# Performance work log

Measured on AMD Instinct MI355X. Metric: run time of the kernel, lower is better.

Reference implementation:

```python
import jax, jax.numpy as jnp
import numpy as np
from jax import lax

B, S, D, H = 64, 256, 512, 8
DH = D // H
FILTER_HEIGHTS = (1, 3, 5)


def setup_inputs() -> dict:
    key = jax.random.key(0)
    ks = jax.random.split(key, 20)
    w = lambda k, shape, s=0.02: (jax.random.normal(k, shape, dtype=jnp.float32) * s)
    inp = {
        "x": jax.random.normal(ks[0], (B, S, D), dtype=jnp.float32),
        "particles": jax.random.uniform(ks[1], (B, S, 3), dtype=jnp.float32),
        # QKV and output projections
        "wq": w(ks[2], (D, D)),
        "wk": w(ks[3], (D, D)),
        "wv": w(ks[4], (D, D)),
        "dense_w": w(ks[5], (D, D)),
        "dense_b": jnp.zeros((D,), jnp.float32),
        # attention-score smoothing convs: kernel (h, S, 1, 1) HWIO, full-width
        "conv1_k": w(ks[6], (1, S, 1, 1)),
        "conv1_b": jnp.zeros((1,), jnp.float32),
        "conv3_k": w(ks[7], (3, S, 1, 1)),
        "conv3_b": jnp.zeros((1,), jnp.float32),
        "conv5_k": w(ks[8], (5, S, 1, 1)),
        "conv5_b": jnp.zeros((1,), jnp.float32),
        # pairwise-feature mask net (1x1 convs == per-pair MLP): 4->8->8->1
        "mw1": w(ks[9], (4, 8), 0.1),
        "mb1": jnp.zeros((8,), jnp.float32),
        "mw2": w(ks[10], (8, 8), 0.1),
        "mb2": jnp.zeros((8,), jnp.float32),
        "mw3": w(ks[11], (8, 1), 0.1),
        "mb3": jnp.zeros((1,), jnp.float32),
    }
    return inp


def _conv_same(x, kern, bias):
    # x: [N, S, S, 1], kern: [h, S, 1, 1] -> [N, S, S, 1], TF 'same' padding, stride 1
    y = lax.conv_general_dilated(x, kern, window_strides=(1, 1), padding="SAME",
                                 dimension_numbers=("NHWC", "HWIO", "NHWC"))
    return y + bias


def _pairwise_features(particles):
    pt, eta, phi = particles[..., 0], particles[..., 1], particles[..., 2]
    pt_i, pt_j = pt[:, :, None], pt[:, None, :]
    d_eta = eta[:, :, None] - eta[:, None, :]
    dp = phi[:, :, None] - phi[:, None, :]
    d_phi = jnp.arctan2(jnp.sin(dp), jnp.cos(dp))
    delta = jnp.sqrt(d_eta ** 2 + d_phi ** 2)
    min_pt = jnp.minimum(pt_i, pt_j)
    kT = min_pt * delta
    z = min_pt / (pt_i + pt_j + 1e-8)
    m2 = jnp.maximum(pt_i ** 2 + pt_j ** 2 - 2.0 * pt_i * pt_j * jnp.cos(d_phi), 1e-8)
    eps = 1e-8
    return jnp.stack([
        jnp.log(jnp.maximum(delta, eps)),
        jnp.log(jnp.maximum(kT, eps)),
        jnp.log(jnp.maximum(z, eps)),
        jnp.log(m2),
    ], axis=-1)  # [B, S, S, 4]


def reference(x, particles, wq, wk, wv, dense_w, dense_b,
              conv1_k, conv1_b, conv3_k, conv3_b, conv5_k, conv5_b,
              mw1, mb1, mw2, mb2, mw3, mb3):
    b = x.shape[0]
    split = lambda t: t.reshape(b, S, H, DH).transpose(0, 2, 1, 3)  # [B,H,S,DH]
    q, k, v = split(x @ wq), split(x @ wk), split(x @ wv)

    scores = jnp.einsum("bhqd,bhkd->bhqk", q, k) / jnp.sqrt(jnp.float32(DH))

    # conv smoothing over score matrices (avg of full-width convs h in {1,3,5})
    xs = scores.reshape(b * H, S, S, 1)
    c1 = _conv_same(xs, conv1_k, conv1_b)
    c3 = _conv_same(xs, conv3_k, conv3_b)
    c5 = _conv_same(xs, conv5_k, conv5_b)
    scores = ((c1 + c3 + c5) / 3.0).reshape(b, H, S, S)

    # pairwise-feature mask (1x1 conv net == per-pair MLP)
    feats = _pairwise_features(particles)               # [B,S,S,4]
    m = jax.nn.relu(feats @ mw1 + mb1)
    m = jax.nn.relu(m @ mw2 + mb2)
    m = (m @ mw3 + mb3)[..., 0]                         # [B,S,S]
    m = jnp.clip(m, -10.0, 10.0)
    scores = scores + m[:, None, :, :]

    weights = jax.nn.softmax(scores, axis=-1)
    attn = jnp.einsum("bhqk,bhkd->bhqd", weights, v)
    concat = attn.transpose(0, 2, 1, 3).reshape(b, S, D)
    return concat @ dense_w + dense_b
```

## Files before the change

### kernel.cpp

```cpp
#include <hip/hip_runtime.h>
#include <hip/hip_bf16.h>
#include <math.h>

#define B   64
#define S   256
#define DD  512
#define H   8
#define DH  64
#define BH  (B*H)

typedef short s16x8 __attribute__((ext_vector_type(8)));
typedef short s16x4 __attribute__((ext_vector_type(4)));
typedef float f32x4 __attribute__((ext_vector_type(4)));

typedef __attribute__((address_space(3))) unsigned int       lds_u32;
typedef __attribute__((address_space(1))) const unsigned int glb_u32;

__device__ __forceinline__ short f2bf(float f) {
    __bf16 h = (__bf16)f;
    union { __bf16 b; short s; } u; u.b = h;
    return u.s;
}

__device__ __forceinline__ void glds16(const void* g, void* l) {
    __builtin_amdgcn_global_load_lds((glb_u32*)g, (lds_u32*)l, 16, 0, 0);
}

__global__ __launch_bounds__(256) void convert_x_kernel(
    const float* __restrict__ x, ushort* __restrict__ xbf)
{
    const int idx = blockIdx.x * 256 + threadIdx.x;
    const float4 f0 = *(const float4*)(x + (size_t)idx * 8);
    const float4 f1 = *(const float4*)(x + (size_t)idx * 8 + 4);
    s16x8 o = { f2bf(f0.x), f2bf(f0.y), f2bf(f0.z), f2bf(f0.w),
                f2bf(f1.x), f2bf(f1.y), f2bf(f1.z), f2bf(f1.w) };
    *(s16x8*)(xbf + (size_t)idx * 8) = o;
}

__global__ __launch_bounds__(256) void transpose_w_kernel(
    const float* __restrict__ wq, const float* __restrict__ wk,
    const float* __restrict__ wv, const float* __restrict__ wd,
    ushort* __restrict__ wt)
{
    __shared__ float tile[32][33];
    const int z = blockIdx.z;
    const float* w = (z == 0) ? wq : (z == 1) ? wk : (z == 2) ? wv : wd;
    const int k0 = blockIdx.y * 32, n0 = blockIdx.x * 32;
    const int tx = threadIdx.x & 31, ty = threadIdx.x >> 5;

    #pragma unroll
    for (int r = 0; r < 32; r += 8)
        tile[ty + r][tx] = w[(size_t)(k0 + ty + r) * DD + n0 + tx];
    __syncthreads();
    #pragma unroll
    for (int r = 0; r < 32; r += 8)
        wt[(size_t)z * DD * DD + (size_t)(n0 + ty + r) * DD + k0 + tx] =
            (ushort)f2bf(tile[tx][ty + r]);
}

__global__ __launch_bounds__(256) void build_toeplitz_frag_kernel(
    const float* __restrict__ c1k, const float* __restrict__ c3k,
    const float* __restrict__ c5k, ushort* __restrict__ btf)
{
    const int idx  = blockIdx.x * 256 + threadIdx.x;
    const int lane = idx & 63;
    const int st   = (idx >> 6) % 40;
    const int n    = idx / (40 * 64);
    const int c    = n * 16 + (lane & 15);
    const int r    = st >> 3;
    const int tb   = (st & 7) * 32 + (lane >> 4) * 8;

    s16x8 o;
    #pragma unroll
    for (int e = 0; e < 8; ++e) {
        const int ki = tb + e - c + 127;
        float val = 0.f;
        if (ki >= 0 && ki < 256) {
            val = c5k[r * 256 + ki];
            if (r >= 1 && r <= 3) val += c3k[(r - 1) * 256 + ki];
            if (r == 2)           val += c1k[ki];
            val *= (1.f / 24.f);
        }
        o[e] = f2bf(val);
    }
    *(s16x8*)(btf + (size_t)idx * 8) = o;
}

__global__ __launch_bounds__(256) void vfrag_repack_kernel(
    const ushort* __restrict__ vbT, ushort* __restrict__ vfrag)
{
    const int idx  = blockIdx.x * 256 + threadIdx.x;
    const int lane = idx & 63;
    const int kk   = (idx >> 6) & 7;
    const int n    = (idx >> 9) & 3;
    const int head = idx >> 11;
    const s16x8 v = *(const s16x8*)(vbT
        + ((size_t)(head * 64 + n * 16 + (lane & 15))) * 256
        + kk * 32 + (lane >> 4) * 8);
    *(s16x8*)(vfrag + (size_t)idx * 8) = v;
}

__global__ __launch_bounds__(256) void gemm_vT_kernel(
    const ushort* __restrict__ A, const ushort* __restrict__ Bt,
    ushort* __restrict__ vo)
{
    __shared__ ushort As[128 * 64];
    __shared__ ushort Bs[128 * 64];

    const int tid  = threadIdx.x;
    const int lane = tid & 63, w = tid >> 6;
    const int l15  = lane & 15, l4 = lane >> 4;
    const int wr   = w >> 1, wc = w & 1;
    const int row0 = blockIdx.y * 128, col0 = blockIdx.x * 128;

    f32x4 acc[4][4];
    #pragma unroll
    for (int mt = 0; mt < 4; ++mt)
        #pragma unroll
        for (int nt = 0; nt < 4; ++nt)
            acc[mt][nt] = (f32x4){0.f, 0.f, 0.f, 0.f};

    const int arow = tid >> 3;
    const int acol = (tid & 7) * 8;
    char* ldsA = (char*)As + (tid >> 6) * 1024;
    char* ldsB = (char*)Bs + (tid >> 6) * 1024;

    for (int k0 = 0; k0 < DD; k0 += 64) {
        #pragma unroll
        for (int i = 0; i < 4; ++i)
            glds16(A  + (size_t)(row0 + arow + 32 * i) * DD + k0 + acol,
                   ldsA + 4096 * i);
        #pragma unroll
        for (int i = 0; i < 4; ++i)
            glds16(Bt + (size_t)(col0 + arow + 32 * i) * DD + k0 + acol,
                   ldsB + 4096 * i);
        __syncthreads();

        #pragma unroll
        for (int kk = 0; kk < 2; ++kk) {
            s16x8 af[4], bf[4];
            #pragma unroll
            for (int mt = 0; mt < 4; ++mt) {
                const int row = wr * 64 + mt * 16 + l15;
                af[mt] = *(const s16x8*)((char*)As + row * 128 + kk * 64 + l4 * 16);
            }
            #pragma unroll
            for (int nt = 0; nt < 4; ++nt) {
                const int col = wc * 64 + nt * 16 + l15;
                bf[nt] = *(const s16x8*)((char*)Bs + col * 128 + kk * 64 + l4 * 16);
            }
            #pragma unroll
            for (int mt = 0; mt < 4; ++mt)
                #pragma unroll
                for (int nt = 0; nt < 4; ++nt)
                    acc[mt][nt] = __builtin_amdgcn_mfma_f32_16x16x32_bf16(
                                      af[mt], bf[nt], acc[mt][nt], 0, 0, 0);
        }
        __syncthreads();
    }

    #pragma unroll
    for (int mt = 0; mt < 4; ++mt)
        #pragma unroll
        for (int nt = 0; nt < 4; ++nt) {
            const int r = row0 + wr * 64 + mt * 16 + l4 * 4;
            const int c = col0 + wc * 64 + nt * 16 + l15;
            const int bb = r >> 8, ss = r & 255;
            const int hh = c >> 6, dd = c & 63;
            s16x4 pk = { f2bf(acc[mt][nt][0]), f2bf(acc[mt][nt][1]),
                         f2bf(acc[mt][nt][2]), f2bf(acc[mt][nt][3]) };
            *(s16x4*)(vo + ((size_t)((bb * H + hh) * DH + dd)) * S + ss) = pk;
        }
}

template<int MODE>
__global__ __launch_bounds__(256) void gemm_swapped_kernel(
    const ushort* __restrict__ WtAll, const ushort* __restrict__ Tok,
    ushort* __restrict__ qo, ushort* __restrict__ ko,
    const float* __restrict__ bias, float* __restrict__ outf)
{
    __shared__ ushort As[128 * 64];
    __shared__ ushort Bs[128 * 64];

    const int tid  = threadIdx.x;
    const int lane = tid & 63, w = tid >> 6;
    const int l15  = lane & 15, l4 = lane >> 4;
    const int wr   = w >> 1, wc = w & 1;
    const int frow0 = blockIdx.y * 128;
    const int trow0 = blockIdx.x * 128;
    const ushort* A = WtAll + (MODE == 0 ? (size_t)blockIdx.z * DD * DD : 0);

    f32x4 acc[4][4];
    #pragma unroll
    for (int mt = 0; mt < 4; ++mt)
        #pragma unroll
        for (int nt = 0; nt < 4; ++nt)
            acc[mt][nt] = (f32x4){0.f, 0.f, 0.f, 0.f};

    const int arow = tid >> 3;
    const int acol = (tid & 7) * 8;
    char* ldsA = (char*)As + (tid >> 6) * 1024;
    char* ldsB = (char*)Bs + (tid >> 6) * 1024;

    for (int k0 = 0; k0 < DD; k0 += 64) {
        #pragma unroll
        for (int i = 0; i < 4; ++i)
            glds16(A   + (size_t)(frow0 + arow + 32 * i) * DD + k0 + acol,
                   ldsA + 4096 * i);
        #pragma unroll
        for (int i = 0; i < 4; ++i)
            glds16(Tok + (size_t)(trow0 + arow + 32 * i) * DD + k0 + acol,
                   ldsB + 4096 * i);
        __syncthreads();

        #pragma unroll
        for (int kk = 0; kk < 2; ++kk) {
            s16x8 af[4], bf[4];
            #pragma unroll
            for (int mt = 0; mt < 4; ++mt) {
                const int row = wr * 64 + mt * 16 + l15;
                af[mt] = *(const s16x8*)((char*)As + row * 128 + kk * 64 + l4 * 16);
            }
            #pragma unroll
            for (int nt = 0; nt < 4; ++nt) {
                const int col = wc * 64 + nt * 16 + l15;
                bf[nt] = *(const s16x8*)((char*)Bs + col * 128 + kk * 64 + l4 * 16);
            }
            #pragma unroll
            for (int mt = 0; mt < 4; ++mt)
                #pragma unroll
                for (int nt = 0; nt < 4; ++nt)
                    acc[mt][nt] = __builtin_amdgcn_mfma_f32_16x16x32_bf16(
                                      af[mt], bf[nt], acc[mt][nt], 0, 0, 0);
        }
        __syncthreads();
    }

    if (MODE == 0) {
        ushort* dst = (blockIdx.z == 0) ? qo : ko;
        #pragma unroll
        for (int mt = 0; mt < 4; ++mt)
            #pragma unroll
            for (int nt = 0; nt < 4; ++nt) {
                const int r = trow0 + wc * 64 + nt * 16 + l15;
                const int c = frow0 + wr * 64 + mt * 16 + l4 * 4;
                const int bb = r >> 8, ss = r & 255;
                const int hh = c >> 6, dd = c & 63;
                s16x4 pk = { f2bf(acc[mt][nt][0]), f2bf(acc[mt][nt][1]),
                             f2bf(acc[mt][nt][2]), f2bf(acc[mt][nt][3]) };
                *(s16x4*)(dst + (((size_t)(bb * H + hh)) * S + ss) * DH + dd) = pk;
            }
    } else {
        #pragma unroll
        for (int mt = 0; mt < 4; ++mt) {
            const int c = frow0 + wr * 64 + mt * 16 + l4 * 4;
            const float4 b4 = *(const float4*)(bias + c);
            #pragma unroll
            for (int nt = 0; nt < 4; ++nt) {
                const int r = trow0 + wc * 64 + nt * 16 + l15;
                float4 o = make_float4(acc[mt][nt][0] + b4.x, acc[mt][nt][1] + b4.y,
                                       acc[mt][nt][2] + b4.z, acc[mt][nt][3] + b4.w);
                *(float4*)(outf + (size_t)r * DD + c) = o;
            }
        }
    }
}

__global__ __launch_bounds__(256) void pairwise_mlp_kernel(
    const float* __restrict__ particles,
    const float* __restrict__ mw1, const float* __restrict__ mb1,
    const float* __restrict__ mw2, const float* __restrict__ mb2,
    const float* __restrict__ mw3, const float* __restrict__ mb3,
    const float* __restrict__ c1b, const float* __restrict__ c3b,
    const float* __restrict__ c5b,
    float* __restrict__ mfrag)
{
    __shared__ float w1[32], b1[8], w2[64], b2[8], w3[8];
    __shared__ float b3s;
    const int tid = threadIdx.x;
    if (tid < 32)                 w1[tid]        = mw1[tid];
    if (tid >= 32 && tid < 40)    b1[tid - 32]   = mb1[tid - 32];
    if (tid >= 64 && tid < 128)   w2[tid - 64]   = mw2[tid - 64];
    if (tid >= 128 && tid < 136)  b2[tid - 128]  = mb2[tid - 128];
    if (tid >= 136 && tid < 144)  w3[tid - 136]  = mw3[tid - 136];
    if (tid == 144)               b3s            = mb3[0];

    const int bi = blockIdx.x;
    const int bb = bi >> 8;
    const float pt_i  = particles[(size_t)bi * 3 + 0];
    const float eta_i = particles[(size_t)bi * 3 + 1];
    const float phi_i = particles[(size_t)bi * 3 + 2];

    const int j = tid;
    const float* pj = particles + ((size_t)(bb * S) + j) * 3;
    const float pt_j = pj[0], eta_j = pj[1], phi_j = pj[2];

    __syncthreads();

    const float d_eta = eta_i - eta_j;
    const float dp    = phi_i - phi_j;
    const float d_phi = dp - 6.28318530717958647692f
                             * rintf(dp * 0.15915494309189533577f);
    const float delta = sqrtf(d_eta * d_eta + d_phi * d_phi);
    const float min_pt = fminf(pt_i, pt_j);
    const float kT = min_pt * delta;
    const float zf = min_pt / (pt_i + pt_j + 1e-8f);
    const float cd = cosf(d_phi);
    const float m2 = fmaxf(pt_i * pt_i + pt_j * pt_j - 2.0f * pt_i * pt_j * cd, 1e-8f);

    const float eps = 1e-8f;
    const float f[4] = { logf(fmaxf(delta, eps)),
                         logf(fmaxf(kT,    eps)),
                         logf(fmaxf(zf,    eps)),
                         logf(m2) };

    float h1[8];
    #pragma unroll
    for (int o = 0; o < 8; ++o) {
        float s = b1[o];
        #pragma unroll
        for (int i4 = 0; i4 < 4; ++i4) s += f[i4] * w1[i4 * 8 + o];
        h1[o] = fmaxf(s, 0.0f);
    }
    float h2[8];
    #pragma unroll
    for (int o = 0; o < 8; ++o) {
        float s = b2[o];
        #pragma unroll
        for (int i8 = 0; i8 < 8; ++i8) s += h1[i8] * w2[i8 * 8 + o];
        h2[o] = fmaxf(s, 0.0f);
    }
    float mv = b3s;
    #pragma unroll
    for (int i8 = 0; i8 < 8; ++i8) mv += h2[i8] * w3[i8];
    mv = fminf(fmaxf(mv, -10.0f), 10.0f);
    mv += (c1b[0] + c3b[0] + c5b[0]) * (1.f / 3.f);

    const int ii     = bi & 255;
    const int chunk2 = ii >> 7;
    const int rem    = ii & 127;
    const int wr     = rem >> 6, rt = (rem >> 4) & 3, l4h = (rem >> 2) & 3, rg = rem & 3;
    const int wc     = j >> 6,   n2 = (j >> 4) & 3,  l15 = j & 15;
    const int lane   = l4h * 16 + l15;
    const int w8     = wr * 4 + wc;
    mfrag[((((size_t)(bb * 2 + chunk2)) * 8 + w8) * 64 + lane) * 64
          + rt * 16 + n2 * 4 + rg] = mv;
}

__global__ __launch_bounds__(512, 4) void fused_mfma_kernel(
    const ushort* __restrict__ q, const ushort* __restrict__ kbuf,
    const ushort* __restrict__ vfrag, const ushort* __restrict__ btf,
    const float* __restrict__ mfrag, ushort* __restrict__ attn)
{
    __shared__ __align__(16) char pool[75776];
    char* SC   = pool;
    char* PB   = pool;
    float* RED = (float*)(pool + 73728);

    const int tid  = threadIdx.x;
    const int lane = tid & 63;
    const int w    = tid >> 6;
    const int wr   = w >> 2, wc = w & 3;
    const int l15  = lane & 15, l4 = lane >> 4;
    const int head = blockIdx.y;
    const int bb   = head >> 3, hh = head & 7;
    const int i0   = blockIdx.x * 128;
    const int cb   = wc * 64;

    {
        const ushort* kb_h = kbuf + (size_t)head * S * DH;
        const ushort* qb_h = q    + (size_t)head * S * DH;
        const int ntiles = 5 - wr;
        const int tg0    = wr * 5;
        f32x4 sacc[4][5];
        #pragma unroll
        for (int mt = 0; mt < 4; ++mt)
            #pragma unroll
            for (int nt = 0; nt < 5; ++nt)
                sacc[mt][nt] = (f32x4){0.f, 0.f, 0.f, 0.f};

        #pragma unroll
        for (int kk = 0; kk < 2; ++kk) {
            s16x8 afr[4];
            #pragma unroll
            for (int mt = 0; mt < 4; ++mt)
                afr[mt] = *(const s16x8*)(kb_h
                          + (size_t)(cb + mt * 16 + l15) * 64 + kk * 32 + 8 * l4);
            #pragma unroll
            for (int nt = 0; nt < 5; ++nt) {
                if (nt < ntiles) {
                    const int qrow = i0 - 8 + (tg0 + nt) * 16 + l15;
                    s16x8 bfr = (s16x8){0,0,0,0,0,0,0,0};
                    if ((unsigned)qrow < (unsigned)S)
                        bfr = *(const s16x8*)(qb_h + (size_t)qrow * 64 + kk * 32 + 8 * l4);
                    #pragma unroll
                    for (int mt = 0; mt < 4; ++mt)
                        sacc[mt][nt] = __builtin_amdgcn_mfma_f32_16x16x32_bf16(
                                           afr[mt], bfr, sacc[mt][nt], 0, 0, 0);
                }
            }
        }
        #pragma unroll
        for (int mt = 0; mt < 4; ++mt)
            #pragma unroll
            for (int nt = 0; nt < 5; ++nt) {
                if (nt < ntiles) {
                    const int row = (tg0 + nt) * 16 + l15;
                    const int t0  = cb + mt * 16 + l4 * 4;
                    s16x4 pk = { f2bf(sacc[mt][nt][0]), f2bf(sacc[mt][nt][1]),
                                 f2bf(sacc[mt][nt][2]), f2bf(sacc[mt][nt][3]) };
                    const int byt = (row * 512 + t0 * 2) ^ ((row & 7) << 4);
                    *(s16x4*)(SC + byt) = pk;
                }
            }
    }
    __syncthreads();

    f32x4 cacc[4][4];
    #pragma unroll
    for (int rt = 0; rt < 4; ++rt)
        #pragma unroll
        for (int n = 0; n < 4; ++n)
            cacc[rt][n] = (f32x4){0.f, 0.f, 0.f, 0.f};

    {
        const ushort* btw = btf + (size_t)(wc * 4) * 40 * 512 + lane * 8;

        s16x8 pb[2][4];
        auto ldB = [&](int st, int slot) {
            #pragma unroll
            for (int i = 0; i < 4; ++i)
                pb[slot][i] = *(const s16x8*)(btw + (size_t)(i * 40 + st) * 512);
        };
        auto convStep = [&](int st, int slot) {
            const int r = st >> 3, kb2 = (st & 7) * 64 + 16 * l4;
            #pragma unroll
            for (int rt = 0; rt < 4; ++rt) {
                const int sr = wr * 64 + rt * 16 + l15 + r + 6;
                const s16x8 afr = *(const s16x8*)(SC + ((sr * 512 + kb2) ^ ((sr & 7) << 4)));
                #pragma unroll
                for (int n = 0; n < 4; ++n)
                    cacc[rt][n] = __builtin_amdgcn_mfma_f32_16x16x32_bf16(
                                      afr, pb[slot][n], cacc[rt][n], 0, 0, 0);
            }
        };

        ldB(0, 0);
        for (int qq = 0; qq < 20; ++qq) {
            const int st = qq * 2;
            ldB(st + 1, 1);
            convStep(st + 0, 0);
            if (st + 2 < 40) ldB(st + 2, 0);
            convStep(st + 1, 1);
        }
    }

    {
        const float* mf = mfrag
            + ((((size_t)(bb * 2 + blockIdx.x)) * 8 + w) * 64 + lane) * 64;
        #pragma unroll
        for (int rt = 0; rt < 4; ++rt)
            #pragma unroll
            for (int n = 0; n < 4; ++n) {
                const float4 mv = *(const float4*)(mf + rt * 16 + n * 4);
                cacc[rt][n][0] += mv.x;
                cacc[rt][n][1] += mv.y;
                cacc[rt][n][2] += mv.z;
                cacc[rt][n][3] += mv.w;
            }
    }

    float rmax[4][4];
    #pragma unroll
    for (int rt = 0; rt < 4; ++rt)
        #pragma unroll
        for (int rg = 0; rg < 4; ++rg) {
            float mx = fmaxf(fmaxf(cacc[rt][0][rg], cacc[rt][1][rg]),
                             fmaxf(cacc[rt][2][rg], cacc[rt][3][rg]));
            mx = fmaxf(mx, __shfl_xor(mx, 1));
            mx = fmaxf(mx, __shfl_xor(mx, 2));
            mx = fmaxf(mx, __shfl_xor(mx, 4));
            mx = fmaxf(mx, __shfl_xor(mx, 8));
            rmax[rt][rg] = mx;
        }
    if (l15 == 0) {
        #pragma unroll
        for (int rt = 0; rt < 4; ++rt)
            #pragma unroll
            for (int rg = 0; rg < 4; ++rg)
                RED[(wr * 64 + rt * 16 + l4 * 4 + rg) * 4 + wc] = rmax[rt][rg];
    }
    __syncthreads();
    #pragma unroll
    for (int rt = 0; rt < 4; ++rt)
        #pragma unroll
        for (int rg = 0; rg < 4; ++rg) {
            const int row = wr * 64 + rt * 16 + l4 * 4 + rg;
            rmax[rt][rg] = fmaxf(fmaxf(RED[row * 4 + 0], RED[row * 4 + 1]),
                                 fmaxf(RED[row * 4 + 2], RED[row * 4 + 3]));
        }
    __syncthreads();

    float rinv[4][4];
    #pragma unroll
    for (int rt = 0; rt < 4; ++rt)
        #pragma unroll
        for (int rg = 0; rg < 4; ++rg) {
            float sm = 0.f;
            #pragma unroll
            for (int n = 0; n < 4; ++n) {
                const float e = __expf(cacc[rt][n][rg] - rmax[rt][rg]);
                cacc[rt][n][rg] = e;
                sm += e;
            }
            sm += __shfl_xor(sm, 1);
            sm += __shfl_xor(sm, 2);
            sm += __shfl_xor(sm, 4);
            sm += __shfl_xor(sm, 8);
            rinv[rt][rg] = sm;
        }
    if (l15 == 0) {
        #pragma unroll
        for (int rt = 0; rt < 4; ++rt)
            #pragma unroll
            for (int rg = 0; rg < 4; ++rg)
                RED[(wr * 64 + rt * 16 + l4 * 4 + rg) * 4 + wc] = rinv[rt][rg];
    }
    __syncthreads();
    #pragma unroll
    for (int rt = 0; rt < 4; ++rt)
        #pragma unroll
        for (int rg = 0; rg < 4; ++rg) {
            const int row = wr * 64 + rt * 16 + l4 * 4 + rg;
            const float tot = (RED[row * 4 + 0] + RED[row * 4 + 1])
                            + (RED[row * 4 + 2] + RED[row * 4 + 3]);
            rinv[rt][rg] = 1.f / tot;
        }
    __syncthreads();

    #pragma unroll
    for (int rt = 0; rt < 4; ++rt)
        #pragma unroll
        for (int n = 0; n < 4; ++n)
            #pragma unroll
            for (int rg = 0; rg < 4; ++rg) {
                const int row = wr * 64 + rt * 16 + l4 * 4 + rg;
                const int col = cb + n * 16 + l15;
                const int byt = (row * 512 + col * 2) ^ ((row & 7) << 4);
                *(short*)(PB + byt) = f2bf(cacc[rt][n][rg] * rinv[rt][rg]);
            }
    __syncthreads();

    const ushort* vf_h = vfrag + (size_t)head * 4 * 8 * 512 + lane * 8;
    f32x4 pacc[4];
    #pragma unroll
    for (int n = 0; n < 4; ++n) pacc[n] = (f32x4){0.f, 0.f, 0.f, 0.f};
    #pragma unroll
    for (int kk = 0; kk < 8; ++kk) {
        const int prow = w * 16 + l15;
        const int byta = (prow * 512 + kk * 64 + 16 * l4) ^ ((prow & 7) << 4);
        const s16x8 pa = *(const s16x8*)(PB + byta);
        #pragma unroll
        for (int n = 0; n < 4; ++n) {
            const s16x8 vb8 = *(const s16x8*)(vf_h + (size_t)(n * 8 + kk) * 512);
            pacc[n] = __builtin_amdgcn_mfma_f32_16x16x32_bf16(pa, vb8, pacc[n], 0, 0, 0);
        }
    }
    #pragma unroll
    for (int n = 0; n < 4; ++n)
        #pragma unroll
        for (int rg = 0; rg < 4; ++rg) {
            const int i = i0 + w * 16 + l4 * 4 + rg;
            const int d = n * 16 + l15;
            attn[(((size_t)bb * S + i) * H + hh) * DH + d] = (ushort)f2bf(pacc[n][rg]);
        }
}

extern "C" void kernel_launch(void* const* d_in, const int* in_sizes, int n_in,
                              void* d_out, int out_size, void* d_ws, size_t ws_size,
                              hipStream_t stream)
{
    (void)in_sizes; (void)n_in; (void)out_size; (void)ws_size;

    const float* x        = (const float*)d_in[0];
    const float* particles= (const float*)d_in[1];
    const float* wq       = (const float*)d_in[2];
    const float* wk       = (const float*)d_in[3];
    const float* wv       = (const float*)d_in[4];
    const float* dense_w  = (const float*)d_in[5];
    const float* dense_b  = (const float*)d_in[6];
    const float* c1k      = (const float*)d_in[7];
    const float* c1b      = (const float*)d_in[8];
    const float* c3k      = (const float*)d_in[9];
    const float* c3b      = (const float*)d_in[10];
    const float* c5k      = (const float*)d_in[11];
    const float* c5b      = (const float*)d_in[12];
    const float* mw1      = (const float*)d_in[13];
    const float* mb1      = (const float*)d_in[14];
    const float* mw2      = (const float*)d_in[15];
    const float* mb2      = (const float*)d_in[16];
    const float* mw3      = (const float*)d_in[17];
    const float* mb3      = (const float*)d_in[18];
    float* out = (float*)d_out;

    ushort* xbf   = (ushort*)d_ws;
    ushort* wt    = xbf   + (size_t)8388608;
    ushort* qb    = wt    + (size_t)1048576;
    ushort* kb    = qb    + (size_t)8388608;
    ushort* vbT   = kb    + (size_t)8388608;
    ushort* attnb = vbT   + (size_t)8388608;
    ushort* btf   = attnb + (size_t)8388608;
    ushort* vfrag = btf   + (size_t)327680;
    float*  mfrag = (float*)(vfrag + (size_t)8388608);

    convert_x_kernel<<<dim3(4096), 256, 0, stream>>>(x, xbf);
    transpose_w_kernel<<<dim3(16, 16, 4), 256, 0, stream>>>(wq, wk, wv, dense_w, wt);
    build_toeplitz_frag_kernel<<<dim3(160), 256, 0, stream>>>(c1k, c3k, c5k, btf);
    pairwise_mlp_kernel<<<dim3(B * S), 256, 0, stream>>>(
        particles, mw1, mb1, mw2, mb2, mw3, mb3, c1b, c3b, c5b, mfrag);

    gemm_swapped_kernel<0><<<dim3(128, 4, 2), 256, 0, stream>>>(
        wt, xbf, qb, kb, nullptr, nullptr);
    gemm_vT_kernel<<<dim3(4, 128), 256, 0, stream>>>(
        xbf, wt + (size_t)2 * DD * DD, vbT);
    vfrag_repack_kernel<<<dim3(4096), 256, 0, stream>>>(vbT, vfrag);

    fused_mfma_kernel<<<dim3(2, BH), 512, 0, stream>>>(
        qb, kb, vfrag, btf, mfrag, attnb);

    gemm_swapped_kernel<1><<<dim3(128, 4), 256, 0, stream>>>(
        wt + (size_t)3 * DD * DD, attnb, nullptr, nullptr, dense_b, out);
}
```

Before: 276.7 us.

## Merge prep kernels, write V directly in fragment layout, raise MFMA priority

Four small preprocessing kernels (x conversion, weight transpose, Toeplitz build, pairwise MLP) become one launch that picks its role from the block index. The V projection GEMM now writes straight into the MFMA fragment layout, which removes the separate repack kernel and one round trip through a full-size intermediate buffer. The conv MFMA loop is also wrapped in s_setprio to favour matrix issue. The trade-offs are a larger, more divergent prep kernel and scattered 8-byte stores in the V GEMM epilogue.

```diff
diff --git a/kernel.cpp b/kernel.cpp
--- a/kernel.cpp
+++ b/kernel.cpp
@@ -26,83 +26,146 @@
     __builtin_amdgcn_global_load_lds((glb_u32*)g, (lds_u32*)l, 16, 0, 0);
 }
 
-__global__ __launch_bounds__(256) void convert_x_kernel(
-    const float* __restrict__ x, ushort* __restrict__ xbf)
-{
-    const int idx = blockIdx.x * 256 + threadIdx.x;
-    const float4 f0 = *(const float4*)(x + (size_t)idx * 8);
-    const float4 f1 = *(const float4*)(x + (size_t)idx * 8 + 4);
-    s16x8 o = { f2bf(f0.x), f2bf(f0.y), f2bf(f0.z), f2bf(f0.w),
-                f2bf(f1.x), f2bf(f1.y), f2bf(f1.z), f2bf(f1.w) };
-    *(s16x8*)(xbf + (size_t)idx * 8) = o;
-}
-
-__global__ __launch_bounds__(256) void transpose_w_kernel(
+__global__ __launch_bounds__(256) void prep_kernel(
+    const float* __restrict__ x, ushort* __restrict__ xbf,
     const float* __restrict__ wq, const float* __restrict__ wk,
     const float* __restrict__ wv, const float* __restrict__ wd,
-    ushort* __restrict__ wt)
+    ushort* __restrict__ wt,
+    const float* __restrict__ c1k, const float* __restrict__ c3k,
+    const float* __restrict__ c5k, ushort* __restrict__ btf,
+    const float* __restrict__ particles,
+    const float* __restrict__ mw1, const float* __restrict__ mb1,
+    const float* __restrict__ mw2, const float* __restrict__ mb2,
+    const float* __restrict__ mw3, const float* __restrict__ mb3,
+    const float* __restrict__ c1b, const float* __restrict__ c3b,
+    const float* __restrict__ c5b,
+    float* __restrict__ mfrag)
 {
     __shared__ float tile[32][33];
-    const int z = blockIdx.z;
-    const float* w = (z == 0) ? wq : (z == 1) ? wk : (z == 2) ? wv : wd;
-    const int k0 = blockIdx.y * 32, n0 = blockIdx.x * 32;
-    const int tx = threadIdx.x & 31, ty = threadIdx.x >> 5;
-
-    #pragma unroll
-    for (int r = 0; r < 32; r += 8)
-        tile[ty + r][tx] = w[(size_t)(k0 + ty + r) * DD + n0 + tx];
-    __syncthreads();
-    #pragma unroll
-    for (int r = 0; r < 32; r += 8)
-        wt[(size_t)z * DD * DD + (size_t)(n0 + ty + r) * DD + k0 + tx] =
-            (ushort)f2bf(tile[tx][ty + r]);
-}
-
-__global__ __launch_bounds__(256) void build_toeplitz_frag_kernel(
-    const float* __restrict__ c1k, const float* __restrict__ c3k,
-    const float* __restrict__ c5k, ushort* __restrict__ btf)
-{
-    const int idx  = blockIdx.x * 256 + threadIdx.x;
-    const int lane = idx & 63;
-    const int st   = (idx >> 6) % 40;
-    const int n    = idx / (40 * 64);
-    const int c    = n * 16 + (lane & 15);
-    const int r    = st >> 3;
-    const int tb   = (st & 7) * 32 + (lane >> 4) * 8;
-
-    s16x8 o;
-    #pragma unroll
-    for (int e = 0; e < 8; ++e) {
-        const int ki = tb + e - c + 127;
-        float val = 0.f;
-        if (ki >= 0 && ki < 256) {
-            val = c5k[r * 256 + ki];
-            if (r >= 1 && r <= 3) val += c3k[(r - 1) * 256 + ki];
-            if (r == 2)           val += c1k[ki];
-            val *= (1.f / 24.f);
-        }
-        o[e] = f2bf(val);
-    }
-    *(s16x8*)(btf + (size_t)idx * 8) = o;
-}
-
-__global__ __launch_bounds__(256) void vfrag_repack_kernel(
-    const ushort* __restrict__ vbT, ushort* __restrict__ vfrag)
-{
-    const int idx  = blockIdx.x * 256 + threadIdx.x;
-    const int lane = idx & 63;
-    const int kk   = (idx >> 6) & 7;
-    const int n    = (idx >> 9) & 3;
-    const int head = idx >> 11;
-    const s16x8 v = *(const s16x8*)(vbT
-        + ((size_t)(head * 64 + n * 16 + (lane & 15))) * 256
-        + kk * 32 + (lane >> 4) * 8);
-    *(s16x8*)(vfrag + (size_t)idx * 8) = v;
+    __shared__ float w1[32], b1[8], w2[64], b2[8], w3[8];
+    __shared__ float b3s;
+
+    const int blk = blockIdx.x;
+    const int tid = threadIdx.x;
+
+    if (blk < 4096) {
+        const int idx = blk * 256 + tid;
+        const float4 f0 = *(const float4*)(x + (size_t)idx * 8);
+        const float4 f1 = *(const float4*)(x + (size_t)idx * 8 + 4);
+        s16x8 o = { f2bf(f0.x), f2bf(f0.y), f2bf(f0.z), f2bf(f0.w),
+                    f2bf(f1.x), f2bf(f1.y), f2bf(f1.z), f2bf(f1.w) };
+        *(s16x8*)(xbf + (size_t)idx * 8) = o;
+    } else if (blk < 5120) {
+        const int rem = blk - 4096;
+        const int z  = rem >> 8;
+        const int k0 = ((rem >> 4) & 15) * 32;
+        const int n0 = (rem & 15) * 32;
+        const float* w = (z == 0) ? wq : (z == 1) ? wk : (z == 2) ? wv : wd;
+        const int tx = tid & 31, ty = tid >> 5;
+        #pragma unroll
+        for (int r = 0; r < 32; r += 8)
+            tile[ty + r][tx] = w[(size_t)(k0 + ty + r) * DD + n0 + tx];
+        __syncthreads();
+        #pragma unroll
+        for (int r = 0; r < 32; r += 8)
+            wt[(size_t)z * DD * DD + (size_t)(n0 + ty + r) * DD + k0 + tx] =
+                (ushort)f2bf(tile[tx][ty + r]);
+    } else if (blk < 5280) {
+        const int idx  = (blk - 5120) * 256 + tid;
+        const int lane = idx & 63;
+        const int st   = (idx >> 6) % 40;
+        const int n    = idx / (40 * 64);
+        const int c    = n * 16 + (lane & 15);
+        const int r    = st >> 3;
+        const int tb   = (st & 7) * 32 + (lane >> 4) * 8;
+        s16x8 o;
+        #pragma unroll
+        for (int e = 0; e < 8; ++e) {
+            const int ki = tb + e - c + 127;
+            float val = 0.f;
+            if (ki >= 0 && ki < 256) {
+                val = c5k[r * 256 + ki];
+                if (r >= 1 && r <= 3) val += c3k[(r - 1) * 256 + ki];
+                if (r == 2)           val += c1k[ki];
+                val *= (1.f / 24.f);
+            }
+            o[e] = f2bf(val);
+        }
+        *(s16x8*)(btf + (size_t)idx * 8) = o;
+    } else {
+        if (tid < 32)                 w1[tid]        = mw1[tid];
+        if (tid >= 32 && tid < 40)    b1[tid - 32]   = mb1[tid - 32];
+        if (tid >= 64 && tid < 128)   w2[tid - 64]   = mw2[tid - 64];
+        if (tid >= 128 && tid < 136)  b2[tid - 128]  = mb2[tid - 128];
+        if (tid >= 136 && tid < 144)  w3[tid - 136]  = mw3[tid - 136];
+        if (tid == 144)               b3s            = mb3[0];
+
+        const int bi = blk - 5280;
+        const int bb = bi >> 8;
+        const float pt_i  = particles[(size_t)bi * 3 + 0];
+        const float eta_i = particles[(size_t)bi * 3 + 1];
+        const float phi_i = particles[(size_t)bi * 3 + 2];
+
+        const int j = tid;
+        const float* pj = particles + ((size_t)(bb * S) + j) * 3;
+        const float pt_j = pj[0], eta_j = pj[1], phi_j = pj[2];
+
+        __syncthreads();
+
+        const float d_eta = eta_i - eta_j;
+        const float dp    = phi_i - phi_j;
+        const float d_phi = dp - 6.28318530717958647692f
+                                 * rintf(dp * 0.15915494309189533577f);
+        const float delta = sqrtf(d_eta * d_eta + d_phi * d_phi);
+        const float min_pt = fminf(pt_i, pt_j);
+        const float kT = min_pt * delta;
+        const float zf = min_pt / (pt_i + pt_j + 1e-8f);
+        const float cd = cosf(d_phi);
+        const float m2 = fmaxf(pt_i * pt_i + pt_j * pt_j - 2.0f * pt_i * pt_j * cd, 1e-8f);
+
+        const float eps = 1e-8f;
+        const float f[4] = { logf(fmaxf(delta, eps)),
+                             logf(fmaxf(kT,    eps)),
+                             logf(fmaxf(zf,    eps)),
+                             logf(m2) };
+
+        float h1[8];
+        #pragma unroll
+        for (int o = 0; o < 8; ++o) {
+            float s = b1[o];
+            #pragma unroll
+            for (int i4 = 0; i4 < 4; ++i4) s += f[i4] * w1[i4 * 8 + o];
+            h1[o] = fmaxf(s, 0.0f);
+        }
+        float h2[8];
+        #pragma unroll
+        for (int o = 0; o < 8; ++o) {
+            float s = b2[o];
+            #pragma unroll
+            for (int i8 = 0; i8 < 8; ++i8) s += h1[i8] * w2[i8 * 8 + o];
+            h2[o] = fmaxf(s, 0.0f);
+        }
+        float mv = b3s;
+        #pragma unroll
+        for (int i8 = 0; i8 < 8; ++i8) mv += h2[i8] * w3[i8];
+        mv = fminf(fmaxf(mv, -10.0f), 10.0f);
+        mv += (c1b[0] + c3b[0] + c5b[0]) * (1.f / 3.f);
+
+        const int ii     = bi & 255;
+        const int chunk2 = ii >> 7;
+        const int rem2   = ii & 127;
+        const int wr     = rem2 >> 6, rt = (rem2 >> 4) & 3, l4h = (rem2 >> 2) & 3, rg = rem2 & 3;
+        const int wc     = j >> 6,   n2 = (j >> 4) & 3,  l15 = j & 15;
+        const int lane   = l4h * 16 + l15;
+        const int w8     = wr * 4 + wc;
+        mfrag[((((size_t)(bb * 2 + chunk2)) * 8 + w8) * 64 + lane) * 64
+              + rt * 16 + n2 * 4 + rg] = mv;
+    }
 }
 
 __global__ __launch_bounds__(256) void gemm_vT_kernel(
     const ushort* __restrict__ A, const ushort* __restrict__ Bt,
-    ushort* __restrict__ vo)
+    ushort* __restrict__ vfrag)
 {
     __shared__ ushort As[128 * 64];
     __shared__ ushort Bs[128 * 64];
@@ -166,10 +229,15 @@
             const int r = row0 + wr * 64 + mt * 16 + l4 * 4;
             const int c = col0 + wc * 64 + nt * 16 + l15;
             const int bb = r >> 8, ss = r & 255;
-            const int hh = c >> 6, dd = c & 63;
+            const int hh = c >> 6;
+            const int head = bb * H + hh;
+            const int n  = (c >> 4) & 3;
+            const int kk = ss >> 5;
+            const int lanep = l15 + 16 * ((ss >> 3) & 3);
+            const int e0 = ss & 7;
             s16x4 pk = { f2bf(acc[mt][nt][0]), f2bf(acc[mt][nt][1]),
                          f2bf(acc[mt][nt][2]), f2bf(acc[mt][nt][3]) };
-            *(s16x4*)(vo + ((size_t)((bb * H + hh) * DH + dd)) * S + ss) = pk;
+            *(s16x4*)(vfrag + ((((size_t)(head * 4 + n)) * 8 + kk) * 64 + lanep) * 8 + e0) = pk;
         }
 }
 
@@ -264,87 +332,6 @@
             }
         }
     }
-}
-
-__global__ __launch_bounds__(256) void pairwise_mlp_kernel(
-    const float* __restrict__ particles,
-    const float* __restrict__ mw1, const float* __restrict__ mb1,
-    const float* __restrict__ mw2, const float* __restrict__ mb2,
-    const float* __restrict__ mw3, const float* __restrict__ mb3,
-    const float* __restrict__ c1b, const float* __restrict__ c3b,
-    const float* __restrict__ c5b,
-    float* __restrict__ mfrag)
-{
-    __shared__ float w1[32], b1[8], w2[64], b2[8], w3[8];
-    __shared__ float b3s;
-    const int tid = threadIdx.x;
-    if (tid < 32)                 w1[tid]        = mw1[tid];
-    if (tid >= 32 && tid < 40)    b1[tid - 32]   = mb1[tid - 32];
-    if (tid >= 64 && tid < 128)   w2[tid - 64]   = mw2[tid - 64];
-    if (tid >= 128 && tid < 136)  b2[tid - 128]  = mb2[tid - 128];
-    if (tid >= 136 && tid < 144)  w3[tid - 136]  = mw3[tid - 136];
-    if (tid == 144)               b3s            = mb3[0];
-
-    const int bi = blockIdx.x;
-    const int bb = bi >> 8;
-    const float pt_i  = particles[(size_t)bi * 3 + 0];
-    const float eta_i = particles[(size_t)bi * 3 + 1];
-    const float phi_i = particles[(size_t)bi * 3 + 2];
-
-    const int j = tid;
-    const float* pj = particles + ((size_t)(bb * S) + j) * 3;
-    const float pt_j = pj[0], eta_j = pj[1], phi_j = pj[2];
-
-    __syncthreads();
-
-    const float d_eta = eta_i - eta_j;
-    const float dp    = phi_i - phi_j;
-    const float d_phi = dp - 6.28318530717958647692f
-                             * rintf(dp * 0.15915494309189533577f);
-    const float delta = sqrtf(d_eta * d_eta + d_phi * d_phi);
-    const float min_pt = fminf(pt_i, pt_j);
-    const float kT = min_pt * delta;
-    const float zf = min_pt / (pt_i + pt_j + 1e-8f);
-    const float cd = cosf(d_phi);
-    const float m2 = fmaxf(pt_i * pt_i + pt_j * pt_j - 2.0f * pt_i * pt_j * cd, 1e-8f);
-
-    const float eps = 1e-8f;
-    const float f[4] = { logf(fmaxf(delta, eps)),
-                         logf(fmaxf(kT,    eps)),
-                         logf(fmaxf(zf,    eps)),
-                         logf(m2) };
-
-    float h1[8];
-    #pragma unroll
-    for (int o = 0; o < 8; ++o) {
-        float s = b1[o];
-        #pragma unroll
-        for (int i4 = 0; i4 < 4; ++i4) s += f[i4] * w1[i4 * 8 + o];
-        h1[o] = fmaxf(s, 0.0f);
-    }
-    float h2[8];
-    #pragma unroll
-    for (int o = 0; o < 8; ++o) {
-        float s = b2[o];
-        #pragma unroll
-        for (int i8 = 0; i8 < 8; ++i8) s += h1[i8] * w2[i8 * 8 + o];
-        h2[o] = fmaxf(s, 0.0f);
-    }
-    float mv = b3s;
-    #pragma unroll
-    for (int i8 = 0; i8 < 8; ++i8) mv += h2[i8] * w3[i8];
-    mv = fminf(fmaxf(mv, -10.0f), 10.0f);
-    mv += (c1b[0] + c3b[0] + c5b[0]) * (1.f / 3.f);
-
-    const int ii     = bi & 255;
-    const int chunk2 = ii >> 7;
-    const int rem    = ii & 127;
-    const int wr     = rem >> 6, rt = (rem >> 4) & 3, l4h = (rem >> 2) & 3, rg = rem & 3;
-    const int wc     = j >> 6,   n2 = (j >> 4) & 3,  l15 = j & 15;
-    const int lane   = l4h * 16 + l15;
-    const int w8     = wr * 4 + wc;
-    mfrag[((((size_t)(bb * 2 + chunk2)) * 8 + w8) * 64 + lane) * 64
-          + rt * 16 + n2 * 4 + rg] = mv;
 }
 
 __global__ __launch_bounds__(512, 4) void fused_mfma_kernel(
@@ -434,6 +421,7 @@
         };
         auto convStep = [&](int st, int slot) {
             const int r = st >> 3, kb2 = (st & 7) * 64 + 16 * l4;
+            __builtin_amdgcn_s_setprio(1);
             #pragma unroll
             for (int rt = 0; rt < 4; ++rt) {
                 const int sr = wr * 64 + rt * 16 + l15 + r + 6;
@@ -443,6 +431,7 @@
                     cacc[rt][n] = __builtin_amdgcn_mfma_f32_16x16x32_bf16(
                                       afr, pb[slot][n], cacc[rt][n], 0, 0, 0);
             }
+            __builtin_amdgcn_s_setprio(0);
         };
 
         ldB(0, 0);
@@ -607,23 +596,20 @@
     ushort* wt    = xbf   + (size_t)8388608;
     ushort* qb    = wt    + (size_t)1048576;
     ushort* kb    = qb    + (size_t)8388608;
-    ushort* vbT   = kb    + (size_t)8388608;
-    ushort* attnb = vbT   + (size_t)8388608;
+    ushort* attnb = kb    + (size_t)8388608;
     ushort* btf   = attnb + (size_t)8388608;
     ushort* vfrag = btf   + (size_t)327680;
     float*  mfrag = (float*)(vfrag + (size_t)8388608);
 
-    convert_x_kernel<<<dim3(4096), 256, 0, stream>>>(x, xbf);
-    transpose_w_kernel<<<dim3(16, 16, 4), 256, 0, stream>>>(wq, wk, wv, dense_w, wt);
-    build_toeplitz_frag_kernel<<<dim3(160), 256, 0, stream>>>(c1k, c3k, c5k, btf);
-    pairwise_mlp_kernel<<<dim3(B * S), 256, 0, stream>>>(
+    prep_kernel<<<dim3(21664), 256, 0, stream>>>(
+        x, xbf, wq, wk, wv, dense_w, wt,
+        c1k, c3k, c5k, btf,
         particles, mw1, mb1, mw2, mb2, mw3, mb3, c1b, c3b, c5b, mfrag);
 
     gemm_swapped_kernel<0><<<dim3(128, 4, 2), 256, 0, stream>>>(
         wt, xbf, qb, kb, nullptr, nullptr);
     gemm_vT_kernel<<<dim3(4, 128), 256, 0, stream>>>(
-        xbf, wt + (size_t)2 * DD * DD, vbT);
-    vfrag_repack_kernel<<<dim3(4096), 256, 0, stream>>>(vbT, vfrag);
+        xbf, wt + (size_t)2 * DD * DD, vfrag);
 
     fused_mfma_kernel<<<dim3(2, BH), 512, 0, stream>>>(
         qb, kb, vfrag, btf, mfrag, attnb);
```

Result: faster. 255.5 us (-7.7%).
